# Optimization experiments

Measured on AMD Instinct MI355X. Metric: run time of the kernel, lower is better.

Reference implementation:

```python
import jax, jax.numpy as jnp
import numpy as np

D = 768
H = 8
HD = D // H
MLP = 3072
EPS = 1e-5


def _ln(x, g, b):
    mu = jnp.mean(x, axis=-1, keepdims=True)
    var = jnp.var(x, axis=-1, keepdims=True)
    return (x - mu) * jax.lax.rsqrt(var + EPS) * g + b


def setup_inputs() -> dict:
    key = jax.random.key(0)
    ks = jax.random.split(key, 20)
    B, N = 4, 2048
    s = 0.02
    inp = {
        "x": jax.random.normal(ks[0], (B, N, D), jnp.float32),
        "position_bias": jax.random.normal(ks[1], (N, N), jnp.float32),
        "wq": jax.random.normal(ks[2], (D, D), jnp.float32) * s,
        "bq": jnp.zeros((D,), jnp.float32),
        "wk": jax.random.normal(ks[3], (D, D), jnp.float32) * s,
        "bk": jnp.zeros((D,), jnp.float32),
        "wv": jax.random.normal(ks[4], (D, D), jnp.float32) * s,
        "bv": jnp.zeros((D,), jnp.float32),
        "wo": jax.random.normal(ks[5], (D, D), jnp.float32) * s,
        "bo": jnp.zeros((D,), jnp.float32),
        "g1": jnp.ones((D,), jnp.float32),
        "b1": jnp.zeros((D,), jnp.float32),
        "g2": jnp.ones((D,), jnp.float32),
        "b2": jnp.zeros((D,), jnp.float32),
        "w_ff1": jax.random.normal(ks[6], (D, MLP), jnp.float32) * s,
        "b_ff1": jnp.zeros((MLP,), jnp.float32),
        "w_ff2": jax.random.normal(ks[7], (MLP, D), jnp.float32) * s,
        "b_ff2": jnp.zeros((D,), jnp.float32),
    }
    return inp


def reference(x, position_bias, wq, bq, wk, bk, wv, bv, wo, bo, g1, b1, g2, b2, w_ff1, b_ff1, w_ff2, b_ff2):
    B, N, _ = x.shape
    scale = HD ** -0.5
    # pre-norm attention
    n1 = _ln(x, g1, b1)
    q = (n1 @ wq + bq).reshape(B, N, H, HD).transpose(0, 2, 1, 3)
    k = (n1 @ wk + bk).reshape(B, N, H, HD).transpose(0, 2, 1, 3)
    v = (n1 @ wv + bv).reshape(B, N, H, HD).transpose(0, 2, 1, 3)
    attn = jnp.einsum('bhqd,bhkd->bhqk', q, k) * scale  # [B,H,N,N]
    attn = attn + position_bias[None, None, :, :]
    attn = jax.nn.softmax(attn, axis=-1)
    out = jnp.einsum('bhqk,bhkd->bhqd', attn, v)
    out = out.transpose(0, 2, 1, 3).reshape(B, N, D)
    out = out @ wo + bo
    x = x + out
    # pre-norm GELU MLP (exact erf gelu, torch default)
    n2 = _ln(x, g2, b2)
    h = jax.nn.gelu(n2 @ w_ff1 + b_ff1, approximate=False)
    x = x + (h @ w_ff2 + b_ff2)
    return x
```

## Files before the change

kernel.cpp:

```cpp
#include <hip/hip_runtime.h>
#include <hip/hip_bf16.h>

#define D 768
#define H 8
#define HD 96
#define MLP 3072
#define NB 2048
#define BATCH 4

typedef __attribute__((ext_vector_type(8))) short short8;
typedef __attribute__((ext_vector_type(4))) short short4v;
typedef __attribute__((ext_vector_type(4))) float f32x4;
typedef __attribute__((ext_vector_type(16))) float f32x16;
typedef __attribute__((ext_vector_type(4))) int int4v;

typedef const __attribute__((address_space(1))) unsigned int gu32;
typedef __attribute__((address_space(3))) unsigned int lu32;

__device__ inline void gload16(const void* g, void* l){
  __builtin_amdgcn_global_load_lds((gu32*)g, (lu32*)l, 16, 0, 0);
}

__device__ inline short f2b(float f){
  __hip_bfloat16 h = __float2bfloat16(f);
  return *reinterpret_cast<short*>(&h);
}
__device__ inline float b2f(short s){
  return __uint_as_float(((unsigned)(unsigned short)s) << 16);
}
__device__ inline float fexp2(float x){ return __builtin_amdgcn_exp2f(x); }

__device__ inline unsigned cvtpk(float lo, float hi){
  unsigned r;
  asm volatile("v_cvt_pk_bf16_f32 %0, %1, %2" : "=v"(r) : "v"(lo), "v"(hi));
  return r;
}

__global__ __launch_bounds__(256) void wtrans(const float* __restrict__ in, short* __restrict__ out, int K, int Nc){
  __shared__ float tile[32][33];
  int bk = blockIdx.x, bn = blockIdx.y;
  int tx = threadIdx.x & 31, ty = threadIdx.x >> 5;
  #pragma unroll
  for (int i=0;i<4;++i)
    tile[ty + i*8][tx] = in[(size_t)(bk*32 + ty + i*8)*Nc + bn*32 + tx];
  __syncthreads();
  #pragma unroll
  for (int i=0;i<4;++i)
    out[(size_t)(bn*32 + ty + i*8)*K + bk*32 + tx] = f2b(tile[tx][ty + i*8]);
}

__global__ __launch_bounds__(256) void bias_cat(const float* __restrict__ bq, const float* __restrict__ bk,
                                                const float* __restrict__ bv, float* __restrict__ o){
  int i = blockIdx.x*256 + threadIdx.x;
  if (i < 768){ o[i]=bq[i]; o[768+i]=bk[i]; o[1536+i]=bv[i]; }
}

__global__ __launch_bounds__(256) void pb_reorg(const float* __restrict__ pb, short* __restrict__ pbT){
  int qt = blockIdx.x, kb = blockIdx.y;
  int t = threadIdx.x;
  int l = t >> 2;
  int vbase = (t & 3) * 8;
  int q = qt*32 + (l & 31);
  int hi = l >> 5;
  const float L2E = 1.4426950408889634f;
  short8 o;
  #pragma unroll
  for (int j=0;j<8;++j){
    int v = vbase + j;
    int r = v & 15, tile = v >> 4;
    int k = kb*64 + tile*32 + 8*(r>>2) + (r&3) + 4*hi;
    o[j] = f2b(pb[(size_t)q*NB + k] * L2E);
  }
  *(short8*)&pbT[(((size_t)(qt*32 + kb))*64 + l)*32 + vbase] = o;
}

__global__ __launch_bounds__(256) void ln_k(const float* __restrict__ X, const float* __restrict__ gg,
                                            const float* __restrict__ bb, short* __restrict__ out){
  int row = blockIdx.x, t = threadIdx.x;
  const float* x = X + (size_t)row*D;
  float v0=x[t], v1=x[t+256], v2=x[t+512];
  float s=v0+v1+v2, ss=v0*v0+v1*v1+v2*v2;
  #pragma unroll
  for (int m=1;m<64;m<<=1){ s += __shfl_xor(s,m); ss += __shfl_xor(ss,m); }
  __shared__ float red[8];
  int w=t>>6, lane=t&63;
  if (!lane){ red[w]=s; red[4+w]=ss; }
  __syncthreads();
  s = red[0]+red[1]+red[2]+red[3];
  ss = red[4]+red[5]+red[6]+red[7];
  float mu = s*(1.f/768.f);
  float inv = rsqrtf(ss*(1.f/768.f) - mu*mu + 1e-5f);
  short* o = out + (size_t)row*D;
  o[t]     = f2b((v0-mu)*inv*gg[t]     + bb[t]);
  o[t+256] = f2b((v1-mu)*inv*gg[t+256] + bb[t+256]);
  o[t+512] = f2b((v2-mu)*inv*gg[t+512] + bb[t+512]);
}

template<int MODE>
__global__ __launch_bounds__(256) void gemm_bt(
    const short* __restrict__ A, const short* __restrict__ Bt,
    const float* __restrict__ bias, const float* __restrict__ resid,
    void* __restrict__ Cout, int Nc, int K)
{
  __shared__ __align__(16) short As[2][128][32];
  __shared__ __align__(16) short Bs[2][128][32];
  int m0 = blockIdx.x*128, n0 = blockIdx.y*128;
  int t = threadIdx.x;
  int lane = t & 63, w = t >> 6;
  int wm = w >> 1, wn = w & 1;
  int r = lane & 15, g = lane >> 4;
  const short* aSrc = A  + (size_t)(m0 + (t>>2))*K + (t&3)*8;
  const short* bSrc = Bt + (size_t)(n0 + (t>>2))*K + (t&3)*8;
  size_t rowK64 = (size_t)64*K;
  int dstOff = w*1024;
  f32x4 acc[4][4] = {};
  int nst = K >> 5;
  gload16(aSrc,          (char*)As + dstOff);
  gload16(aSrc + rowK64, (char*)As + 4096 + dstOff);
  gload16(bSrc,          (char*)Bs + dstOff);
  gload16(bSrc + rowK64, (char*)Bs + 4096 + dstOff);
  for (int it=0; it<nst; ++it){
    int cur = it & 1;
    if (it+1 < nst){
      int kt = (it+1)*32;
      char* ab = (char*)As + (cur^1)*8192;
      char* bb = (char*)Bs + (cur^1)*8192;
      gload16(aSrc + kt,          ab + dstOff);
      gload16(aSrc + kt + rowK64, ab + 4096 + dstOff);
      gload16(bSrc + kt,          bb + dstOff);
      gload16(bSrc + kt + rowK64, bb + 4096 + dstOff);
      asm volatile("s_waitcnt vmcnt(4)" ::: "memory");
    } else {
      asm volatile("s_waitcnt vmcnt(0)" ::: "memory");
    }
    __builtin_amdgcn_s_barrier();
    __builtin_amdgcn_sched_barrier(0);
    short8 af[4], bfr[4];
    #pragma unroll
    for (int i=0;i<4;++i){
      af[i]  = *(const short8*)&As[cur][wm*64 + i*16 + r][g*8];
      bfr[i] = *(const short8*)&Bs[cur][wn*64 + i*16 + r][g*8];
    }
    #pragma unroll
    for (int i=0;i<4;++i)
      #pragma unroll
      for (int j=0;j<4;++j)
        acc[i][j] = __builtin_amdgcn_mfma_f32_16x16x32_bf16(af[i], bfr[j], acc[i][j], 0,0,0);
    __builtin_amdgcn_sched_barrier(0);
    __builtin_amdgcn_s_barrier();
  }
  #pragma unroll
  for (int i=0;i<4;++i){
    #pragma unroll
    for (int j=0;j<4;++j){
      int col = n0 + wn*64 + j*16 + r;
      float bv = bias[col];
      #pragma unroll
      for (int q=0;q<4;++q){
        int row = m0 + wm*64 + i*16 + g*4 + q;
        size_t idx = (size_t)row*Nc + col;
        float val = acc[i][j][q] + bv;
        if constexpr (MODE==0){
          ((short*)Cout)[idx] = f2b(val);
        } else if constexpr (MODE==2){
          float ge = 0.5f*val*(1.f + erff(val*0.70710678118654752f));
          ((short*)Cout)[idx] = f2b(ge);
        }
      }
    }
  }
}

template<int MODE>
__global__ __launch_bounds__(256) void gemm64(
    const short* __restrict__ A, const short* __restrict__ Bt,
    const float* __restrict__ bias, const float* __restrict__ resid,
    void* __restrict__ Cout, int Nc, int K)
{
  __shared__ __align__(16) short As[2][64][32];
  __shared__ __align__(16) short Bs[2][128][32];
  int m0 = blockIdx.x*64, n0 = blockIdx.y*128;
  int t = threadIdx.x;
  int lane = t & 63, w = t >> 6;
  int r = lane & 15, g = lane >> 4;
  const short* aSrc = A  + (size_t)(m0 + (t>>2))*K + (t&3)*8;
  const short* bSrc = Bt + (size_t)(n0 + (t>>2))*K + (t&3)*8;
  size_t rowK64 = (size_t)64*K;
  int dstOff = w*1024;
  f32x4 acc[4][2] = {};
  int nst = K >> 5;
  gload16(aSrc,          (char*)As + dstOff);
  gload16(bSrc,          (char*)Bs + dstOff);
  gload16(bSrc + rowK64, (char*)Bs + 4096 + dstOff);
  for (int it=0; it<nst; ++it){
    int cur = it & 1;
    if (it+1 < nst){
      int kt = (it+1)*32;
      char* ab = (char*)As + (cur^1)*4096;
      char* bb = (char*)Bs + (cur^1)*8192;
      gload16(aSrc + kt,          ab + dstOff);
      gload16(bSrc + kt,          bb + dstOff);
      gload16(bSrc + kt + rowK64, bb + 4096 + dstOff);
      asm volatile("s_waitcnt vmcnt(3)" ::: "memory");
    } else {
      asm volatile("s_waitcnt vmcnt(0)" ::: "memory");
    }
    __builtin_amdgcn_s_barrier();
    __builtin_amdgcn_sched_barrier(0);
    short8 af[4], bfr[2];
    #pragma unroll
    for (int i=0;i<4;++i) af[i] = *(const short8*)&As[cur][i*16 + r][g*8];
    #pragma unroll
    for (int j=0;j<2;++j) bfr[j] = *(const short8*)&Bs[cur][w*32 + j*16 + r][g*8];
    #pragma unroll
    for (int i=0;i<4;++i)
      #pragma unroll
      for (int j=0;j<2;++j)
        acc[i][j] = __builtin_amdgcn_mfma_f32_16x16x32_bf16(af[i], bfr[j], acc[i][j], 0,0,0);
    __builtin_amdgcn_sched_barrier(0);
    __builtin_amdgcn_s_barrier();
  }
  #pragma unroll
  for (int i=0;i<4;++i){
    #pragma unroll
    for (int j=0;j<2;++j){
      int col = n0 + w*32 + j*16 + r;
      #pragma unroll
      for (int q=0;q<4;++q){
        int row = m0 + i*16 + g*4 + q;
        if constexpr (MODE==1){
          size_t idx = (size_t)row*Nc + col;
          ((float*)Cout)[idx] = acc[i][j][q] + bias[col] + resid[idx];
        } else {
          int hh = row / 96, hd = row - hh*96;
          int bb = col >> 11, nn = col & 2047;
          size_t idx = ((size_t)((bb*8 + hh)*96 + hd))*2048 + nn;
          ((short*)Cout)[idx] = f2b(acc[i][j][q] + bias[row]);
        }
      }
    }
  }
}

__global__ __launch_bounds__(512, 1) void attn_k(const short* __restrict__ qkv, const short* __restrict__ v_t,
                                                 const short* __restrict__ pbT, short* __restrict__ aout){
  int bx = blockIdx.x;
  int h = bx & 7, b = (bx>>3)&3, qb = bx>>5;
  int t = threadIdx.x, l = t & 63, w = t >> 6;
  int l31 = l & 31, hi = l >> 5, l7 = l & 7;
  __shared__ __align__(16) short Ks[2][64][128];
  __shared__ __align__(16) short Vs[96][64];
  const float SCALE2 = 0.10206207261596575f * 1.4426950408889634f;

  int qRow = qb*256 + w*32 + l31;
  const short* qg = qkv + (size_t)(b*NB + qRow)*1536 + h*HD;
  short8 qa[6];
  #pragma unroll
  for (int ds=0; ds<6; ++ds)
    qa[ds] = *(const short8*)&qg[ds*16 + hi*8];

  f32x16 oacc[3] = {};
  float m_run = -3.0e38f, l_run = 0.f;

  int r0 = t/12,        c0 = t%12;
  int s1 = 512 + t;
  int r1 = s1/12,       c1 = s1%12;
  int ldsK0 = r0*128 + (c0 ^ (r0&7))*8;
  int ldsK1 = r1*128 + (c1 ^ (r1&7))*8;
  const short* kgB = qkv + (size_t)(b*NB)*1536 + 768 + h*HD;
  bool wlow = (t < 256);
  int vr0 = t>>3,  vc0 = t&7;
  int vr1 = (512+t)>>3, vc1 = (512+t)&7;
  const short* vgB = v_t + (size_t)((b*H+h)*HD)*NB;
  const short* vsrc0 = vgB + (size_t)vr0*NB + (vc0 ^ (vr0&7))*8;
  const short* vsrc1 = vgB + (size_t)vr1*NB + (vc1 ^ (vr1&7))*8;
  char* vdst0 = (char*)Vs + w*1024;
  char* vdst1 = (char*)Vs + 8192 + w*1024;
  const short* pbB = pbT + (((size_t)((qb*8 + w)*32))*64 + l)*32;

  {
    short8 ka = *(const short8*)&kgB[(size_t)r0*1536 + c0*8];
    short* ks0 = &Ks[0][0][0];
    *(short8*)(ks0 + ldsK0) = ka;
    if (wlow){
      short8 kb = *(const short8*)&kgB[(size_t)r1*1536 + c1*8];
      *(short8*)(ks0 + ldsK1) = kb;
    }
  }
  __syncthreads();

  for (int kt=0; kt<32; ++kt){
    int cur = kt & 1;
    int kbase = kt*64;
    const short* pbk = pbB + kt*2048;
    short8 pbr0 = *(const short8*)&pbk[0];
    short8 pbr1 = *(const short8*)&pbk[8];
    short8 pbr2 = *(const short8*)&pbk[16];
    short8 pbr3 = *(const short8*)&pbk[24];
    gload16(vsrc0 + kbase, vdst0);
    if (wlow) gload16(vsrc1 + kbase, vdst1);
    int kb2 = (kt < 31) ? (kbase + 64) : kbase;
    short8 kra = *(const short8*)&kgB[(size_t)(kb2 + r0)*1536 + c0*8];
    short8 krb = {};
    if (wlow) krb = *(const short8*)&kgB[(size_t)(kb2 + r1)*1536 + c1*8];

    f32x16 sacc[2] = {};
    __builtin_amdgcn_s_setprio(1);
    #pragma unroll
    for (int tt=0; tt<2; ++tt){
      #pragma unroll
      for (int ds=0; ds<6; ++ds){
        short8 kf = *(const short8*)&Ks[cur][tt*32 + l31][((ds*2 + hi) ^ l7)*8];
        sacc[tt] = __builtin_amdgcn_mfma_f32_32x32x16_bf16(kf, qa[ds], sacc[tt], 0,0,0);
      }
    }
    __builtin_amdgcn_s_setprio(0);

    float vals[2][16];
    #pragma unroll
    for (int tt=0; tt<2; ++tt)
      #pragma unroll
      for (int r=0; r<16; ++r){
        int v = tt*16 + r;
        short pv = (v<8)?pbr0[v]:(v<16)?pbr1[v-8]:(v<24)?pbr2[v-16]:pbr3[v-24];
        vals[tt][r] = fmaf(sacc[tt][r], SCALE2, b2f(pv));
      }
    float pm = vals[0][0];
    #pragma unroll
    for (int tt=0; tt<2; ++tt)
      #pragma unroll
      for (int r=0; r<16; ++r) pm = fmaxf(pm, vals[tt][r]);
    pm = fmaxf(pm, __shfl_xor(pm, 32));
    if (__any(pm - m_run > 8.f)){
      float mn = fmaxf(m_run, pm);
      float f = fexp2(m_run - mn);
      l_run *= f; m_run = mn;
      int fi = __float_as_int(f);
      #pragma unroll
      for (int reg=0; reg<16; ++reg){
        int q = (reg&3) + 8*(reg>>2) + 4*hi;
        float fr = __int_as_float(__builtin_amdgcn_ds_bpermute(q<<2, fi));
        oacc[0][reg] *= fr; oacc[1][reg] *= fr; oacc[2][reg] *= fr;
      }
    }
    float p[2][16];
    float rs = 0.f;
    #pragma unroll
    for (int tt=0; tt<2; ++tt)
      #pragma unroll
      for (int r=0; r<16; ++r){
        p[tt][r] = fexp2(vals[tt][r] - m_run);
        rs += p[tt][r];
      }
    rs += __shfl_xor(rs, 32);
    l_run += rs;

    short8 pa[4];
    #pragma unroll
    for (int ks=0; ks<4; ++ks){
      int tt = ks>>1;
      int rb = (ks&1)*8;
      unsigned G0a = cvtpk(p[tt][rb+0], p[tt][rb+1]);
      unsigned G0b = cvtpk(p[tt][rb+2], p[tt][rb+3]);
      unsigned G1a = cvtpk(p[tt][rb+4], p[tt][rb+5]);
      unsigned G1b = cvtpk(p[tt][rb+6], p[tt][rb+7]);
      unsigned sG0a = (unsigned)__shfl_xor((int)G0a, 32);
      unsigned sG0b = (unsigned)__shfl_xor((int)G0b, 32);
      unsigned sG1a = (unsigned)__shfl_xor((int)G1a, 32);
      unsigned sG1b = (unsigned)__shfl_xor((int)G1b, 32);
      int4v wv;
      wv[0] = hi ? (int)sG1a : (int)G0a;
      wv[1] = hi ? (int)sG1b : (int)G0b;
      wv[2] = hi ? (int)G1a  : (int)sG0a;
      wv[3] = hi ? (int)G1b  : (int)sG0b;
      pa[ks] = __builtin_bit_cast(short8, wv);
    }

    __syncthreads();

    __builtin_amdgcn_s_setprio(1);
    #pragma unroll
    for (int dt=0; dt<3; ++dt){
      #pragma unroll
      for (int ks=0; ks<4; ++ks){
        short8 vb = *(const short8*)&Vs[dt*32 + l31][((ks*2 + hi) ^ l7)*8];
        oacc[dt] = __builtin_amdgcn_mfma_f32_32x32x16_bf16(pa[ks], vb, oacc[dt], 0,0,0);
      }
    }
    __builtin_amdgcn_s_setprio(0);

    if (kt < 31){
      short* ksn = &Ks[cur^1][0][0];
      *(short8*)(ksn + ldsK0) = kra;
      if (wlow) *(short8*)(ksn + ldsK1) = krb;
      __syncthreads();
    }
  }

  float inv_self = 1.f / l_run;
  int ii = __float_as_int(inv_self);
  #pragma unroll
  for (int reg=0; reg<16; ++reg){
    int q = (reg&3) + 8*(reg>>2) + 4*hi;
    float invq = __int_as_float(__builtin_amdgcn_ds_bpermute(q<<2, ii));
    int rowg = b*NB + qb*256 + w*32 + q;
    #pragma unroll
    for (int dt=0; dt<3; ++dt){
      int col = h*HD + dt*32 + l31;
      aout[(size_t)rowg*D + col] = f2b(oacc[dt][reg] * invq);
    }
  }
}

extern "C" void kernel_launch(void* const* d_in, const int* in_sizes, int n_in,
                              void* d_out, int out_size, void* d_ws, size_t ws_size,
                              hipStream_t stream){
  const float* x   = (const float*)d_in[0];
  const float* pb  = (const float*)d_in[1];
  const float* wq  = (const float*)d_in[2];
  const float* bq  = (const float*)d_in[3];
  const float* wk  = (const float*)d_in[4];
  const float* bk  = (const float*)d_in[5];
  const float* wv  = (const float*)d_in[6];
  const float* bv  = (const float*)d_in[7];
  const float* wo  = (const float*)d_in[8];
  const float* bo  = (const float*)d_in[9];
  const float* g1  = (const float*)d_in[10];
  const float* b1  = (const float*)d_in[11];
  const float* g2  = (const float*)d_in[12];
  const float* b2  = (const float*)d_in[13];
  const float* wf1 = (const float*)d_in[14];
  const float* bf1 = (const float*)d_in[15];
  const float* wf2 = (const float*)d_in[16];
  const float* bf2 = (const float*)d_in[17];
  float* out = (float*)d_out;

  char* p = (char*)d_ws;
  auto alloc = [&](size_t bytes){ char* q = p; p += (bytes + 255) & ~(size_t)255; return q; };
  short* wqkv_t = (short*)alloc((size_t)2304*768*2);
  short* wo_t   = (short*)alloc((size_t)768*768*2);
  short* w1_t   = (short*)alloc((size_t)3072*768*2);
  short* w2_t   = (short*)alloc((size_t)768*3072*2);
  float* bqkv   = (float*)alloc(2304*4);
  short* pbT    = (short*)alloc((size_t)2048*2048*2);
  float* x1     = (float*)alloc((size_t)8192*768*4);
  short* n2     = (short*)alloc((size_t)8192*768*2);
  short* n1     = (short*)alloc((size_t)8192*768*2);
  short* qkv    = (short*)alloc((size_t)8192*1536*2);
  short* v_t    = (short*)alloc((size_t)32*96*2048*2);
  short* hbuf   = n1;
  short* attn_o = n1;
  short* wv_t   = wqkv_t + (size_t)2*768*768;

  wtrans<<<dim3(24,24),256,0,stream>>>(wq, wqkv_t,           768, 768);
  wtrans<<<dim3(24,24),256,0,stream>>>(wk, wqkv_t + 768*768, 768, 768);
  wtrans<<<dim3(24,24),256,0,stream>>>(wv, wv_t,             768, 768);
  wtrans<<<dim3(24,24),256,0,stream>>>(wo, wo_t, 768, 768);
  wtrans<<<dim3(24,96),256,0,stream>>>(wf1, w1_t, 768, 3072);
  wtrans<<<dim3(96,24),256,0,stream>>>(wf2, w2_t, 3072, 768);
  bias_cat<<<3,256,0,stream>>>(bq,bk,bv,bqkv);
  pb_reorg<<<dim3(64,32),256,0,stream>>>(pb, pbT);
  ln_k<<<8192,256,0,stream>>>(x, g1, b1, n1);
  gemm_bt<0><<<dim3(64,12),256,0,stream>>>(n1, wqkv_t, bqkv, nullptr, qkv, 1536, 768);
  gemm64<5><<<dim3(12,64),256,0,stream>>>(wv_t, n1, bv, nullptr, v_t, 0, 768);
  attn_k<<<256,512,0,stream>>>(qkv, v_t, pbT, attn_o);
  gemm64<1><<<dim3(128,6),256,0,stream>>>(attn_o, wo_t, bo, x, x1, 768, 768);
  ln_k<<<8192,256,0,stream>>>(x1, g2, b2, n2);
  gemm_bt<2><<<dim3(64,24),256,0,stream>>>(n2, w1_t, bf1, nullptr, hbuf, 3072, 768);
  gemm64<1><<<dim3(128,6),256,0,stream>>>(hbuf, w2_t, bf2, x1, out, 768, 3072);
}
```

Baseline: 324.9 us.

## Triple-buffer GEMM shared tiles and double-buffer V tiles in attention

Both GEMM kernels go from a double-buffered shared-memory ring to a three-deep ring. Each iteration prefetches tile it+2 right after a single barrier, and the trailing barrier per K-step is dropped. The attention kernel now double-buffers the V tile: the next tile's async load is issued during the current iteration, and the __syncthreads before the PV MFMAs is removed. The aim is to cut barrier stalls and hide global-load latency, at the cost of more LDS per block, which could lower occupancy.

```diff
diff --git a/kernel.cpp b/kernel.cpp
--- a/kernel.cpp
+++ b/kernel.cpp
@@ -102,8 +102,8 @@
     const float* __restrict__ bias, const float* __restrict__ resid,
     void* __restrict__ Cout, int Nc, int K)
 {
-  __shared__ __align__(16) short As[2][128][32];
-  __shared__ __align__(16) short Bs[2][128][32];
+  __shared__ __align__(16) short As[3][128][32];
+  __shared__ __align__(16) short Bs[3][128][32];
   int m0 = blockIdx.x*128, n0 = blockIdx.y*128;
   int t = threadIdx.x;
   int lane = t & 63, w = t >> 6;
@@ -115,26 +115,26 @@
   int dstOff = w*1024;
   f32x4 acc[4][4] = {};
   int nst = K >> 5;
-  gload16(aSrc,          (char*)As + dstOff);
-  gload16(aSrc + rowK64, (char*)As + 4096 + dstOff);
-  gload16(bSrc,          (char*)Bs + dstOff);
-  gload16(bSrc + rowK64, (char*)Bs + 4096 + dstOff);
+  auto stage = [&](int u, int buf){
+    char* ab = (char*)As + buf*8192;
+    char* bb = (char*)Bs + buf*8192;
+    int kt = u*32;
+    gload16(aSrc + kt,          ab + dstOff);
+    gload16(aSrc + kt + rowK64, ab + 4096 + dstOff);
+    gload16(bSrc + kt,          bb + dstOff);
+    gload16(bSrc + kt + rowK64, bb + 4096 + dstOff);
+  };
+  stage(0,0); stage(1,1);
+  int cur = 0;
   for (int it=0; it<nst; ++it){
-    int cur = it & 1;
-    if (it+1 < nst){
-      int kt = (it+1)*32;
-      char* ab = (char*)As + (cur^1)*8192;
-      char* bb = (char*)Bs + (cur^1)*8192;
-      gload16(aSrc + kt,          ab + dstOff);
-      gload16(aSrc + kt + rowK64, ab + 4096 + dstOff);
-      gload16(bSrc + kt,          bb + dstOff);
-      gload16(bSrc + kt + rowK64, bb + 4096 + dstOff);
-      asm volatile("s_waitcnt vmcnt(4)" ::: "memory");
-    } else {
-      asm volatile("s_waitcnt vmcnt(0)" ::: "memory");
-    }
+    if (it < nst-1) asm volatile("s_waitcnt vmcnt(4)" ::: "memory");
+    else            asm volatile("s_waitcnt vmcnt(0)" ::: "memory");
     __builtin_amdgcn_s_barrier();
     __builtin_amdgcn_sched_barrier(0);
+    if (it+2 < nst){
+      int sb = cur+2; if (sb>=3) sb-=3;
+      stage(it+2, sb);
+    }
     short8 af[4], bfr[4];
     #pragma unroll
     for (int i=0;i<4;++i){
@@ -146,8 +146,7 @@
       #pragma unroll
       for (int j=0;j<4;++j)
         acc[i][j] = __builtin_amdgcn_mfma_f32_16x16x32_bf16(af[i], bfr[j], acc[i][j], 0,0,0);
-    __builtin_amdgcn_sched_barrier(0);
-    __builtin_amdgcn_s_barrier();
+    cur = cur+1; if (cur>=3) cur-=3;
   }
   #pragma unroll
   for (int i=0;i<4;++i){
@@ -177,8 +176,8 @@
     const float* __restrict__ bias, const float* __restrict__ resid,
     void* __restrict__ Cout, int Nc, int K)
 {
-  __shared__ __align__(16) short As[2][64][32];
-  __shared__ __align__(16) short Bs[2][128][32];
+  __shared__ __align__(16) short As[3][64][32];
+  __shared__ __align__(16) short Bs[3][128][32];
   int m0 = blockIdx.x*64, n0 = blockIdx.y*128;
   int t = threadIdx.x;
   int lane = t & 63, w = t >> 6;
@@ -189,24 +188,25 @@
   int dstOff = w*1024;
   f32x4 acc[4][2] = {};
   int nst = K >> 5;
-  gload16(aSrc,          (char*)As + dstOff);
-  gload16(bSrc,          (char*)Bs + dstOff);
-  gload16(bSrc + rowK64, (char*)Bs + 4096 + dstOff);
+  auto stage = [&](int u, int buf){
+    char* ab = (char*)As + buf*4096;
+    char* bb = (char*)Bs + buf*8192;
+    int kt = u*32;
+    gload16(aSrc + kt,          ab + dstOff);
+    gload16(bSrc + kt,          bb + dstOff);
+    gload16(bSrc + kt + rowK64, bb + 4096 + dstOff);
+  };
+  stage(0,0); stage(1,1);
+  int cur = 0;
   for (int it=0; it<nst; ++it){
-    int cur = it & 1;
-    if (it+1 < nst){
-      int kt = (it+1)*32;
-      char* ab = (char*)As + (cur^1)*4096;
-      char* bb = (char*)Bs + (cur^1)*8192;
-      gload16(aSrc + kt,          ab + dstOff);
-      gload16(bSrc + kt,          bb + dstOff);
-      gload16(bSrc + kt + rowK64, bb + 4096 + dstOff);
-      asm volatile("s_waitcnt vmcnt(3)" ::: "memory");
-    } else {
-      asm volatile("s_waitcnt vmcnt(0)" ::: "memory");
-    }
+    if (it < nst-1) asm volatile("s_waitcnt vmcnt(3)" ::: "memory");
+    else            asm volatile("s_waitcnt vmcnt(0)" ::: "memory");
     __builtin_amdgcn_s_barrier();
     __builtin_amdgcn_sched_barrier(0);
+    if (it+2 < nst){
+      int sb = cur+2; if (sb>=3) sb-=3;
+      stage(it+2, sb);
+    }
     short8 af[4], bfr[2];
     #pragma unroll
     for (int i=0;i<4;++i) af[i] = *(const short8*)&As[cur][i*16 + r][g*8];
@@ -217,8 +217,7 @@
       #pragma unroll
       for (int j=0;j<2;++j)
         acc[i][j] = __builtin_amdgcn_mfma_f32_16x16x32_bf16(af[i], bfr[j], acc[i][j], 0,0,0);
-    __builtin_amdgcn_sched_barrier(0);
-    __builtin_amdgcn_s_barrier();
+    cur = cur+1; if (cur>=3) cur-=3;
   }
   #pragma unroll
   for (int i=0;i<4;++i){
@@ -249,7 +248,7 @@
   int t = threadIdx.x, l = t & 63, w = t >> 6;
   int l31 = l & 31, hi = l >> 5, l7 = l & 7;
   __shared__ __align__(16) short Ks[2][64][128];
-  __shared__ __align__(16) short Vs[96][64];
+  __shared__ __align__(16) short Vs[2][96][64];
   const float SCALE2 = 0.10206207261596575f * 1.4426950408889634f;
 
   int qRow = qb*256 + w*32 + l31;
@@ -274,8 +273,6 @@
   const short* vgB = v_t + (size_t)((b*H+h)*HD)*NB;
   const short* vsrc0 = vgB + (size_t)vr0*NB + (vc0 ^ (vr0&7))*8;
   const short* vsrc1 = vgB + (size_t)vr1*NB + (vc1 ^ (vr1&7))*8;
-  char* vdst0 = (char*)Vs + w*1024;
-  char* vdst1 = (char*)Vs + 8192 + w*1024;
   const short* pbB = pbT + (((size_t)((qb*8 + w)*32))*64 + l)*32;
 
   {
@@ -286,23 +283,28 @@
       short8 kb = *(const short8*)&kgB[(size_t)r1*1536 + c1*8];
       *(short8*)(ks0 + ldsK1) = kb;
     }
+    gload16(vsrc0, (char*)Vs + w*1024);
+    if (wlow) gload16(vsrc1, (char*)Vs + 8192 + w*1024);
   }
   __syncthreads();
 
   for (int kt=0; kt<32; ++kt){
     int cur = kt & 1;
     int kbase = kt*64;
+    int kb2 = (kt < 31) ? (kbase + 64) : kbase;
+    short8 kra = *(const short8*)&kgB[(size_t)(kb2 + r0)*1536 + c0*8];
+    short8 krb = {};
+    if (wlow) krb = *(const short8*)&kgB[(size_t)(kb2 + r1)*1536 + c1*8];
     const short* pbk = pbB + kt*2048;
     short8 pbr0 = *(const short8*)&pbk[0];
     short8 pbr1 = *(const short8*)&pbk[8];
     short8 pbr2 = *(const short8*)&pbk[16];
     short8 pbr3 = *(const short8*)&pbk[24];
-    gload16(vsrc0 + kbase, vdst0);
-    if (wlow) gload16(vsrc1 + kbase, vdst1);
-    int kb2 = (kt < 31) ? (kbase + 64) : kbase;
-    short8 kra = *(const short8*)&kgB[(size_t)(kb2 + r0)*1536 + c0*8];
-    short8 krb = {};
-    if (wlow) krb = *(const short8*)&kgB[(size_t)(kb2 + r1)*1536 + c1*8];
+    if (kt < 31){
+      char* vbd = (char*)Vs + (cur^1)*12288;
+      gload16(vsrc0 + kbase + 64, vbd + w*1024);
+      if (wlow) gload16(vsrc1 + kbase + 64, vbd + 8192 + w*1024);
+    }
 
     f32x16 sacc[2] = {};
     __builtin_amdgcn_s_setprio(1);
@@ -376,14 +378,12 @@
       pa[ks] = __builtin_bit_cast(short8, wv);
     }
 
-    __syncthreads();
-
     __builtin_amdgcn_s_setprio(1);
     #pragma unroll
     for (int dt=0; dt<3; ++dt){
       #pragma unroll
       for (int ks=0; ks<4; ++ks){
-        short8 vb = *(const short8*)&Vs[dt*32 + l31][((ks*2 + hi) ^ l7)*8];
+        short8 vb = *(const short8*)&Vs[cur][dt*32 + l31][((ks*2 + hi) ^ l7)*8];
         oacc[dt] = __builtin_amdgcn_mfma_f32_32x32x16_bf16(pa[ks], vb, oacc[dt], 0,0,0);
       }
     }
```

New measurement: 318.7 us. Within noise of the previous version (-1.9%).
